# Performance work log

Measured on AMD Instinct MI355X. Metric: run time of the kernel, lower is better.

The kernel has to match this reference:

```python
import jax, jax.numpy as jnp
import numpy as np

GROUPS = 256   # B: number of index groups
SEQ = 512      # L: tokens per group (equal-length groups)
D_IN = 128
D_QK = 64
D_V = 128


def setup_inputs() -> dict:
    key = jax.random.key(0)
    ks = jax.random.split(key, 7)
    N = GROUPS * SEQ
    inputs = jax.random.normal(ks[0], (N, D_IN), dtype=jnp.float32)
    # sorted group ids: GROUPS groups of SEQ tokens each
    index = jnp.repeat(jnp.arange(GROUPS, dtype=jnp.int64), SEQ)
    s_in = 1.0 / np.sqrt(D_IN)
    Wq = jax.random.normal(ks[1], (D_IN, D_QK), dtype=jnp.float32) * s_in
    bq = jax.random.normal(ks[2], (D_QK,), dtype=jnp.float32) * 0.01
    Wk = jax.random.normal(ks[3], (D_IN, D_QK), dtype=jnp.float32) * s_in
    bk = jax.random.normal(ks[4], (D_QK,), dtype=jnp.float32) * 0.01
    Wv = jax.random.normal(ks[5], (D_IN, D_V), dtype=jnp.float32) * s_in
    bv = jax.random.normal(ks[6], (D_V,), dtype=jnp.float32) * 0.01
    return {"inputs": inputs, "index": index, "Wq": Wq, "bq": bq,
            "Wk": Wk, "bk": bk, "Wv": Wv, "bv": bv}


def reference(inputs, index, Wq, bq, Wk, bk, Wv, bv):
    # Linear projections on flat tokens [N, d]
    q = inputs @ Wq + bq          # [N, D_QK]
    k = inputs @ Wk + bk          # [N, D_QK]
    v = inputs @ Wv + bv          # [N, D_V]
    # unbatch: equal-length sorted groups -> [B, L, d]
    q = q.reshape(GROUPS, SEQ, D_QK)
    k = k.reshape(GROUPS, SEQ, D_QK)
    v = v.reshape(GROUPS, SEQ, D_V)
    # note the module's scale: sqrt(2 * d_qk)
    scale = 1.0 / np.sqrt(2.0 * D_QK).astype(np.float32)
    scores = jnp.einsum('bqd,bkd->bqk', q, k) * scale   # [B, L, L]
    attn = jax.nn.softmax(scores, axis=-1)
    out = jnp.einsum('bqk,bkd->bqd', attn, v)           # [B, L, D_V]
    return out.reshape(-1, D_V)                          # [N, D_V]
```

## Files before the change

### kernel.cpp

```cpp
#include <hip/hip_runtime.h>
#include <hip/hip_bf16.h>
#include <stdint.h>

#define GROUPS 256
#define SEQ    512
#define D_IN   128
#define D_QK   64
#define D_V    128
#define NTOK   (GROUPS * SEQ)

#define SL2E (0.08838834764831845f * 1.4426950408889634f)

typedef short bf8 __attribute__((ext_vector_type(8)));
typedef short bf4 __attribute__((ext_vector_type(4)));
typedef float f32x4 __attribute__((ext_vector_type(4)));

__device__ __forceinline__ short f2bf(float f) {
    __bf16 h = (__bf16)f;
    return __builtin_bit_cast(short, h);
}

__device__ __forceinline__ void gload_lds16(const void* g, void* l) {
    __builtin_amdgcn_global_load_lds(
        (const __attribute__((address_space(1))) unsigned int*)(uintptr_t)(g),
        (__attribute__((address_space(3))) unsigned int*)(uint32_t)(uintptr_t)(l),
        16, 0, 0);
}

__global__ __launch_bounds__(256) void prep_w(
    const float* __restrict__ Wq, const float* __restrict__ bq,
    const float* __restrict__ Wk, const float* __restrict__ bk,
    const float* __restrict__ Wv, const float* __restrict__ bv,
    short* __restrict__ Wt, float* __restrict__ bcat)
{
    const int t = blockIdx.x * 256 + threadIdx.x;
    const int r  = t >> 5;
    const int k0 = (t & 31) * 4;
    const float* W; int ld; int c; float sc;
    if (r < 64)       { W = Wq; ld = 64;  c = r;       sc = SL2E; }
    else if (r < 128) { W = Wk; ld = 64;  c = r - 64;  sc = 1.0f; }
    else              { W = Wv; ld = 128; c = r - 128; sc = 1.0f; }
    bf4 pk;
#pragma unroll
    for (int i = 0; i < 4; ++i) pk[i] = f2bf(W[(size_t)(k0 + i) * ld + c] * sc);
    const int phys = (k0 * 2) ^ ((r & 7) << 4);
    *reinterpret_cast<bf4*>((char*)Wt + r * 256 + phys) = pk;
    if (t < 256) {
        const float* b = (t < 64) ? bq : (t < 128 ? bk : bv);
        const int cb   = (t < 64) ? t  : (t < 128 ? t - 64 : t - 128);
        bcat[t] = b[cb] * (t < 64 ? SL2E : 1.0f);
    }
}

__global__ __launch_bounds__(256) void proj_kernel(
    const float* __restrict__ x, const short* __restrict__ Wt,
    const float* __restrict__ bcat,
    short* __restrict__ Q, short* __restrict__ K, short* __restrict__ Vt)
{
    __shared__ short wlds[32768];
    const int tid = threadIdx.x;
    const int wid = tid >> 6, lane = tid & 63, l15 = lane & 15, lg = lane >> 4;

#pragma unroll
    for (int i = 0; i < 16; ++i)
        gload_lds16((const char*)Wt + i * 4096 + tid * 16,
                    (char*)wlds + i * 4096 + tid * 16);

    const size_t tw = (size_t)blockIdx.x * 256 + wid * 64;
    const int g     = (int)(tw >> 9);
    const int tseg  = (int)(tw & 511);

    bf8 xf[4][4];
#pragma unroll
    for (int m = 0; m < 4; ++m) {
        const float* xr = x + (tw + m * 16 + l15) * D_IN;
#pragma unroll
        for (int kf = 0; kf < 4; ++kf) {
            const float4 a = *reinterpret_cast<const float4*>(xr + kf * 32 + lg * 8);
            const float4 b = *reinterpret_cast<const float4*>(xr + kf * 32 + lg * 8 + 4);
            bf8 v;
            v[0] = f2bf(a.x); v[1] = f2bf(a.y); v[2] = f2bf(a.z); v[3] = f2bf(a.w);
            v[4] = f2bf(b.x); v[5] = f2bf(b.y); v[6] = f2bf(b.z); v[7] = f2bf(b.w);
            xf[m][kf] = v;
        }
    }
    __syncthreads();

#pragma unroll
    for (int cf = 0; cf < 16; ++cf) {
        const int wrow = cf * 16 + l15;
        bf8 wf[4];
#pragma unroll
        for (int kf = 0; kf < 4; ++kf) {
            const int off = (kf * 64 + lg * 16) ^ ((wrow & 7) << 4);
            wf[kf] = *reinterpret_cast<const bf8*>((const char*)wlds + wrow * 256 + off);
        }

        if (cf < 8) {
            const float4 bias4 = *reinterpret_cast<const float4*>(bcat + cf * 16 + lg * 4);
#pragma unroll
            for (int m = 0; m < 4; ++m) {
                f32x4 acc = (f32x4){0.f, 0.f, 0.f, 0.f};
#pragma unroll
                for (int kf = 0; kf < 4; ++kf)
                    acc = __builtin_amdgcn_mfma_f32_16x16x32_bf16(wf[kf], xf[m][kf], acc, 0, 0, 0);
                bf4 pk;
                pk[0] = f2bf(acc[0] + bias4.x); pk[1] = f2bf(acc[1] + bias4.y);
                pk[2] = f2bf(acc[2] + bias4.z); pk[3] = f2bf(acc[3] + bias4.w);
                const size_t tok = tw + m * 16 + l15;
                if (cf < 4) {
                    *reinterpret_cast<bf4*>((char*)Q + tok * 128 + cf * 32 + lg * 8) = pk;
                } else {
                    const int lo = ((cf - 4) * 32 + lg * 8) ^ (((int)tok & 7) << 4);
                    *reinterpret_cast<bf4*>((char*)K + tok * 128 + lo) = pk;
                }
            }
        } else {
            const int d = (cf - 8) * 16 + l15;
            const float bias = bcat[cf * 16 + l15];
            char* vrow = (char*)Vt + (((size_t)g * D_V + d) << 10);
            const int sd = (d >> 1) & 3;
#pragma unroll
            for (int m = 0; m < 4; ++m) {
                f32x4 acc = (f32x4){0.f, 0.f, 0.f, 0.f};
#pragma unroll
                for (int kf = 0; kf < 4; ++kf)
                    acc = __builtin_amdgcn_mfma_f32_16x16x32_bf16(xf[m][kf], wf[kf], acc, 0, 0, 0);
                bf4 pk;
#pragma unroll
                for (int r = 0; r < 4; ++r) pk[r] = f2bf(acc[r] + bias);
                const int t0   = tseg + m * 16;
                const int phys = (t0 >> 5) * 64 + ((lg ^ sd) << 4) + ((t0 >> 4) & 1) * 8;
                *reinterpret_cast<bf4*>(vrow + phys) = pk;
            }
        }
    }
}

__global__ __launch_bounds__(256, 4) void attn_kernel(
    const short* __restrict__ Q, const short* __restrict__ K,
    const short* __restrict__ Vt, float* __restrict__ out)
{
    __shared__ short lds[2 * 6144];
    const int g = blockIdx.x, rb = blockIdx.y;
    const int tid = threadIdx.x, wid = tid >> 6, lane = tid & 63;
    const int l15 = lane & 15, lg = lane >> 4;
    const size_t gtok = (size_t)g * SEQ;
    const int row0 = rb * 128 + wid * 32;

    bf8 qf[2][2];
#pragma unroll
    for (int rf = 0; rf < 2; ++rf) {
        const short* qr = Q + (gtok + row0 + rf * 16 + l15) * 64 + lg * 8;
        qf[rf][0] = *reinterpret_cast<const bf8*>(qr);
        qf[rf][1] = *reinterpret_cast<const bf8*>(qr + 32);
    }

    const char* Kg = (const char*)(K + gtok * 64);
    const char* Vg = (const char*)(Vt + ((size_t)g * D_V << 9));

    f32x4 o[2][8];
#pragma unroll
    for (int rf = 0; rf < 2; ++rf)
#pragma unroll
        for (int vt = 0; vt < 8; ++vt) o[rf][vt] = (f32x4){0.f, 0.f, 0.f, 0.f};
    f32x4 psv[2] = {(f32x4){0.f, 0.f, 0.f, 0.f}, (f32x4){0.f, 0.f, 0.f, 0.f}};
    const bf8 onesf = {0x3F80, 0x3F80, 0x3F80, 0x3F80, 0x3F80, 0x3F80, 0x3F80, 0x3F80};

    auto stage = [&](int kt, int b) {
        char* lbase = (char*)lds + b * 12288;
        int c = wid * 3;
#pragma unroll
        for (int i = 0; i < 3; ++i, ++c) {
            if (c < 4) {
                gload_lds16(Kg + (size_t)kt * 4096 + c * 1024 + lane * 16,
                            lbase + c * 1024 + lane * 16);
            } else {
                const int cv = c - 4;
                const int d  = cv * 16 + (lane >> 2);
                gload_lds16(Vg + (size_t)d * 1024 + kt * 64 + (lane & 3) * 16,
                            lbase + 4096 + cv * 1024 + lane * 16);
            }
        }
    };

    auto compute = [&](int b) {
        const char* lb = (const char*)lds + b * 12288;
        f32x4 st[2][2];
#pragma unroll
        for (int tf = 0; tf < 2; ++tf) {
            const int tok = tf * 16 + l15;
            const char* kb = lb + tok * 128;
            const int x7 = (tok & 7) << 4;
            const bf8 k0 = *reinterpret_cast<const bf8*>(kb + ((lg * 16) ^ x7));
            const bf8 k1 = *reinterpret_cast<const bf8*>(kb + ((64 + lg * 16) ^ x7));
#pragma unroll
            for (int rf = 0; rf < 2; ++rf) {
                f32x4 s = (f32x4){0.f, 0.f, 0.f, 0.f};
                s = __builtin_amdgcn_mfma_f32_16x16x32_bf16(k0, qf[rf][0], s, 0, 0, 0);
                s = __builtin_amdgcn_mfma_f32_16x16x32_bf16(k1, qf[rf][1], s, 0, 0, 0);
                st[tf][rf] = s;
            }
        }
        bf8 pa[2];
#pragma unroll
        for (int rf = 0; rf < 2; ++rf) {
            bf8 pv;
#pragma unroll
            for (int i = 0; i < 4; ++i) {
                pv[i]     = f2bf(__builtin_amdgcn_exp2f(st[0][rf][i]));
                pv[i + 4] = f2bf(__builtin_amdgcn_exp2f(st[1][rf][i]));
            }
            pa[rf] = pv;
            psv[rf] = __builtin_amdgcn_mfma_f32_16x16x32_bf16(pv, onesf, psv[rf], 0, 0, 0);
        }
        const char* vb = lb + 4096;
#pragma unroll
        for (int vt = 0; vt < 8; ++vt) {
            const int d = vt * 16 + l15;
            const char* vr = vb + d * 64;
            const bf8 v0 = *reinterpret_cast<const bf8*>(vr + ((lg * 16) ^ ((((d >> 1) & 3)) << 4)));
            o[0][vt] = __builtin_amdgcn_mfma_f32_16x16x32_bf16(pa[0], v0, o[0][vt], 0, 0, 0);
            o[1][vt] = __builtin_amdgcn_mfma_f32_16x16x32_bf16(pa[1], v0, o[1][vt], 0, 0, 0);
        }
    };

    stage(0, 0);
    __syncthreads();
    for (int kt = 0; kt < 16; ++kt) {
        const int b = kt & 1;
        if (kt < 15) stage(kt + 1, b ^ 1);
        compute(b);
        __syncthreads();
    }

#pragma unroll
    for (int rf = 0; rf < 2; ++rf) {
        float linv[4];
#pragma unroll
        for (int r = 0; r < 4; ++r) linv[r] = 1.0f / psv[rf][r];
        float* op = out + (gtok + row0 + rf * 16) * D_V;
#pragma unroll
        for (int vt = 0; vt < 8; ++vt)
#pragma unroll
            for (int r = 0; r < 4; ++r)
                op[(size_t)(lg * 4 + r) * D_V + vt * 16 + l15] = o[rf][vt][r] * linv[r];
    }
}

extern "C" void kernel_launch(void* const* d_in, const int* in_sizes, int n_in,
                              void* d_out, int out_size, void* d_ws, size_t ws_size,
                              hipStream_t stream) {
    (void)in_sizes; (void)n_in; (void)ws_size; (void)out_size;
    const float* x  = (const float*)d_in[0];
    const float* Wq = (const float*)d_in[2];
    const float* bq = (const float*)d_in[3];
    const float* Wk = (const float*)d_in[4];
    const float* bk = (const float*)d_in[5];
    const float* Wv = (const float*)d_in[6];
    const float* bv = (const float*)d_in[7];
    float* out = (float*)d_out;

    short* Qw = (short*)d_ws;
    short* Kw = Qw + (size_t)NTOK * D_QK;
    short* Vt = Kw + (size_t)NTOK * D_QK;

    short* Wt   = (short*)out;
    float* bcat = (float*)((char*)out + 65536);

    prep_w<<<32, 256, 0, stream>>>(Wq, bq, Wk, bk, Wv, bv, Wt, bcat);
    proj_kernel<<<NTOK / 256, 256, 0, stream>>>(x, Wt, bcat, Qw, Kw, Vt);
    attn_kernel<<<dim3(GROUPS, 4), 256, 0, stream>>>(Qw, Kw, Vt, out);
}
```

Before: 75.60 us.

## Restructure projection: stage x tile in LDS, keep weight slices in registers per wave

The projection kernel now handles 64 tokens per block instead of 256. Each block stages the fp32 input tile into LDS with swizzled async global-to-LDS loads, and each wave keeps a fixed quarter of the weight rows (Q, K, or two V slices) in registers, read straight from global memory. The whole weight matrix is no longer copied into LDS per block, and every wave shares the same x tile rather than loading its own tokens. The trade-off is four times as many blocks, with each re-reading weight fragments from global/L2 memory, and wave-level divergence in work type (Q/K vs V output layout).

```diff
diff --git a/kernel.cpp b/kernel.cpp
--- a/kernel.cpp
+++ b/kernel.cpp
@@ -43,8 +43,7 @@
     bf4 pk;
 #pragma unroll
     for (int i = 0; i < 4; ++i) pk[i] = f2bf(W[(size_t)(k0 + i) * ld + c] * sc);
-    const int phys = (k0 * 2) ^ ((r & 7) << 4);
-    *reinterpret_cast<bf4*>((char*)Wt + r * 256 + phys) = pk;
+    *reinterpret_cast<bf4*>(Wt + r * 128 + k0) = pk;
     if (t < 256) {
         const float* b = (t < 64) ? bq : (t < 128 ? bk : bv);
         const int cb   = (t < 64) ? t  : (t < 128 ? t - 64 : t - 128);
@@ -57,81 +56,87 @@
     const float* __restrict__ bcat,
     short* __restrict__ Q, short* __restrict__ K, short* __restrict__ Vt)
 {
-    __shared__ short wlds[32768];
+    __shared__ float xs[8192];
     const int tid = threadIdx.x;
     const int wid = tid >> 6, lane = tid & 63, l15 = lane & 15, lg = lane >> 4;
-
-#pragma unroll
-    for (int i = 0; i < 16; ++i)
-        gload_lds16((const char*)Wt + i * 4096 + tid * 16,
-                    (char*)wlds + i * 4096 + tid * 16);
-
-    const size_t tw = (size_t)blockIdx.x * 256 + wid * 64;
-    const int g     = (int)(tw >> 9);
-    const int tseg  = (int)(tw & 511);
-
-    bf8 xf[4][4];
+    const size_t tb = (size_t)blockIdx.x * 64;
+    const int g    = (int)(tb >> 9);
+    const int tseg = (int)(tb & 511);
+
+#pragma unroll
+    for (int i = 0; i < 8; ++i) {
+        const int cph  = i * 256 + tid;
+        const int tok  = cph >> 5;
+        const int lchk = (cph & 31) ^ (tok & 7);
+        gload_lds16((const char*)(x + (tb + tok) * D_IN) + lchk * 16,
+                    (char*)xs + cph * 16);
+    }
+
+    bf8 wf[4][4];
+#pragma unroll
+    for (int q = 0; q < 4; ++q) {
+        const int cf = wid * 4 + q;
+        const short* wr = Wt + (cf * 16 + l15) * 128 + lg * 8;
+#pragma unroll
+        for (int kf = 0; kf < 4; ++kf)
+            wf[q][kf] = *reinterpret_cast<const bf8*>(wr + kf * 32);
+    }
+    __syncthreads();
+
 #pragma unroll
     for (int m = 0; m < 4; ++m) {
-        const float* xr = x + (tw + m * 16 + l15) * D_IN;
+        const int tl = m * 16 + l15;
+        const int sx = tl & 7;
+        bf8 xfm[4];
 #pragma unroll
         for (int kf = 0; kf < 4; ++kf) {
-            const float4 a = *reinterpret_cast<const float4*>(xr + kf * 32 + lg * 8);
-            const float4 b = *reinterpret_cast<const float4*>(xr + kf * 32 + lg * 8 + 4);
+            const int c0 = (kf * 8 + lg * 2) ^ sx;
+            const int c1 = (kf * 8 + lg * 2 + 1) ^ sx;
+            const f32x4 a = *reinterpret_cast<const f32x4*>((const char*)xs + tl * 512 + c0 * 16);
+            const f32x4 b = *reinterpret_cast<const f32x4*>((const char*)xs + tl * 512 + c1 * 16);
             bf8 v;
-            v[0] = f2bf(a.x); v[1] = f2bf(a.y); v[2] = f2bf(a.z); v[3] = f2bf(a.w);
-            v[4] = f2bf(b.x); v[5] = f2bf(b.y); v[6] = f2bf(b.z); v[7] = f2bf(b.w);
-            xf[m][kf] = v;
-        }
-    }
-    __syncthreads();
-
-#pragma unroll
-    for (int cf = 0; cf < 16; ++cf) {
-        const int wrow = cf * 16 + l15;
-        bf8 wf[4];
-#pragma unroll
-        for (int kf = 0; kf < 4; ++kf) {
-            const int off = (kf * 64 + lg * 16) ^ ((wrow & 7) << 4);
-            wf[kf] = *reinterpret_cast<const bf8*>((const char*)wlds + wrow * 256 + off);
-        }
-
-        if (cf < 8) {
-            const float4 bias4 = *reinterpret_cast<const float4*>(bcat + cf * 16 + lg * 4);
-#pragma unroll
-            for (int m = 0; m < 4; ++m) {
+            v[0] = f2bf(a[0]); v[1] = f2bf(a[1]); v[2] = f2bf(a[2]); v[3] = f2bf(a[3]);
+            v[4] = f2bf(b[0]); v[5] = f2bf(b[1]); v[6] = f2bf(b[2]); v[7] = f2bf(b[3]);
+            xfm[kf] = v;
+        }
+
+        if (wid < 2) {
+#pragma unroll
+            for (int q = 0; q < 4; ++q) {
+                const int cf = wid * 4 + q;
                 f32x4 acc = (f32x4){0.f, 0.f, 0.f, 0.f};
 #pragma unroll
                 for (int kf = 0; kf < 4; ++kf)
-                    acc = __builtin_amdgcn_mfma_f32_16x16x32_bf16(wf[kf], xf[m][kf], acc, 0, 0, 0);
+                    acc = __builtin_amdgcn_mfma_f32_16x16x32_bf16(wf[q][kf], xfm[kf], acc, 0, 0, 0);
+                const float4 bias4 = *reinterpret_cast<const float4*>(bcat + cf * 16 + lg * 4);
                 bf4 pk;
                 pk[0] = f2bf(acc[0] + bias4.x); pk[1] = f2bf(acc[1] + bias4.y);
                 pk[2] = f2bf(acc[2] + bias4.z); pk[3] = f2bf(acc[3] + bias4.w);
-                const size_t tok = tw + m * 16 + l15;
-                if (cf < 4) {
-                    *reinterpret_cast<bf4*>((char*)Q + tok * 128 + cf * 32 + lg * 8) = pk;
+                const size_t tok = tb + tl;
+                if (wid == 0) {
+                    *reinterpret_cast<bf4*>((char*)Q + tok * 128 + q * 32 + lg * 8) = pk;
                 } else {
-                    const int lo = ((cf - 4) * 32 + lg * 8) ^ (((int)tok & 7) << 4);
+                    const int lo = (q * 32 + lg * 8) ^ (((int)tok & 7) << 4);
                     *reinterpret_cast<bf4*>((char*)K + tok * 128 + lo) = pk;
                 }
             }
         } else {
-            const int d = (cf - 8) * 16 + l15;
-            const float bias = bcat[cf * 16 + l15];
-            char* vrow = (char*)Vt + (((size_t)g * D_V + d) << 10);
-            const int sd = (d >> 1) & 3;
-#pragma unroll
-            for (int m = 0; m < 4; ++m) {
+#pragma unroll
+            for (int q = 0; q < 4; ++q) {
+                const int cf = wid * 4 + q;
                 f32x4 acc = (f32x4){0.f, 0.f, 0.f, 0.f};
 #pragma unroll
                 for (int kf = 0; kf < 4; ++kf)
-                    acc = __builtin_amdgcn_mfma_f32_16x16x32_bf16(xf[m][kf], wf[kf], acc, 0, 0, 0);
+                    acc = __builtin_amdgcn_mfma_f32_16x16x32_bf16(xfm[kf], wf[q][kf], acc, 0, 0, 0);
+                const int d = (cf - 8) * 16 + l15;
+                const float bias = bcat[cf * 16 + l15];
                 bf4 pk;
 #pragma unroll
                 for (int r = 0; r < 4; ++r) pk[r] = f2bf(acc[r] + bias);
                 const int t0   = tseg + m * 16;
+                const int sd   = (d >> 1) & 3;
                 const int phys = (t0 >> 5) * 64 + ((lg ^ sd) << 4) + ((t0 >> 4) & 1) * 8;
-                *reinterpret_cast<bf4*>(vrow + phys) = pk;
+                *reinterpret_cast<bf4*>((char*)Vt + (((size_t)g * D_V + d) << 10) + phys) = pk;
             }
         }
     }
@@ -269,6 +274,6 @@
     float* bcat = (float*)((char*)out + 65536);
 
     prep_w<<<32, 256, 0, stream>>>(Wq, bq, Wk, bk, Wv, bv, Wt, bcat);
-    proj_kernel<<<NTOK / 256, 256, 0, stream>>>(x, Wt, bcat, Qw, Kw, Vt);
+    proj_kernel<<<NTOK / 64, 256, 0, stream>>>(x, Wt, bcat, Qw, Kw, Vt);
     attn_kernel<<<dim3(GROUPS, 4), 256, 0, stream>>>(Qw, Kw, Vt, out);
 }
```

Result: slower. 88.31 us (+16.8%).
